# Kernel optimization log

Hardware: AMD Instinct MI355X
Metric: run time of the kernel (lower is better)

The kernel has to match this reference:

```python
import jax, jax.numpy as jnp
import numpy as np

N = 10000        # nodes
E = 320000       # edges (avg degree 32)
W = 256          # width (assert width >= 256)
H = 8            # num_head (RESCALE_EDGE assumed (1,1) -> nhead=8, dhead=32)
D = W // H       # per-head dim
BOND = 33        # EMBED_BOND[0]
BAG = 3          # indices per edge bag
EPS_GN = 1e-5


def setup_inputs() -> dict:
    key = jax.random.key(0)
    ks = jax.random.split(key, 12)
    x = jax.random.normal(ks[0], (N, W), dtype=jnp.float32)
    edge_idx = jax.random.randint(ks[1], (2, E), 0, N)
    edge_attr = jax.random.randint(ks[2], (E, BAG), 0, BOND)
    # node in-degree wrt scatter target edge_idx[1], clamped to >= 1
    deg = jax.ops.segment_sum(jnp.ones((E,), jnp.float32), edge_idx[1], num_segments=N)
    deg = jnp.maximum(deg, 1.0)
    s = 1.0 / np.sqrt(W)
    W_src = jax.random.normal(ks[3], (W, W), dtype=jnp.float32) * s
    W_tgt = jax.random.normal(ks[4], (W, W), dtype=jnp.float32) * s
    emb = jax.random.normal(ks[5], (BOND, W), dtype=jnp.float32) * 0.02
    emb = emb.at[0].set(0.0)  # padding_idx=0 row is zeros
    sd = 1.0 / np.sqrt(D)
    W_gate = jax.random.normal(ks[6], (H, D, D), dtype=jnp.float32) * sd  # grouped conv1d k=1
    W_val = jax.random.normal(ks[7], (H, D, D), dtype=jnp.float32) * sd
    W_post = jax.random.normal(ks[8], (W, W), dtype=jnp.float32) * s
    deg_param = jnp.zeros((W,), jnp.float32) - 0.01  # DegreeLayer degree_init
    return {"x": x, "deg": deg, "edge_idx": edge_idx, "edge_attr": edge_attr,
            "W_src": W_src, "W_tgt": W_tgt, "emb": emb,
            "W_gate": W_gate, "W_val": W_val, "W_post": W_post,
            "deg_param": deg_param}


def reference(x, deg, edge_idx, edge_attr, W_src, W_tgt, emb, W_gate, W_val, W_post, deg_param):
    # src/tgt 1x1 Conv1d == per-node linear, then edge gather
    xs = x @ W_src.T                      # [N, W]
    xt = x @ W_tgt.T                      # [N, W]
    xx = xs[edge_idx[0]] + xt[edge_idx[1]]  # [E, W]

    # EmbeddingBag(mode='mean', padding_idx=0): padded entries excluded
    mask = (edge_attr != 0).astype(xx.dtype)            # [E, BAG]
    bag = jnp.einsum('ebc,eb->ec', emb[edge_attr], mask)  # [E, W]
    cnt = jnp.maximum(mask.sum(-1, keepdims=True), 1.0)
    gate_bias = bag / cnt

    # GroupNorm(H, W, affine=False) over [E, W, 1]
    xg = xx.reshape(-1, H, D)
    mu = xg.mean(-1, keepdims=True)
    var = xg.var(-1, keepdims=True)
    xn = (xg - mu) / jnp.sqrt(var + EPS_GN)              # [E, H, D]

    # gated grouped 1x1 convs (dropout is identity at eval)
    gin = xn + gate_bias.reshape(-1, H, D)
    gate = jax.nn.relu(jnp.einsum('ehd,hfd->ehf', gin, W_gate))
    val = jnp.einsum('ehd,hfd->ehf', xn, W_val)
    act = (gate * val).reshape(-1, W)                    # [E, W]
    out_e = act @ W_post.T                               # [E, W]

    # scatter-sum to nodes, then degree rescale
    agg = jax.ops.segment_sum(out_e, edge_idx[1], num_segments=x.shape[0])
    return jnp.power(deg[:, None], deg_param) * agg      # [N, W]
```

## Files before the change

kernel.cpp:

```cpp
#include <hip/hip_runtime.h>

#define WID 256
#define EPS_GN 1e-5f

typedef __bf16 v8bf __attribute__((ext_vector_type(8)));
typedef __bf16 v2bf __attribute__((ext_vector_type(2)));
typedef float  v4f  __attribute__((ext_vector_type(4)));
typedef float  v2f  __attribute__((ext_vector_type(2)));

__device__ inline unsigned short f2b(float f) {
    unsigned int u = __builtin_bit_cast(unsigned int, f);
    unsigned int r = (u + 0x7fffu + ((u >> 16) & 1u)) >> 16;
    return (unsigned short)r;
}
__device__ inline float lo16(unsigned int u) { return __builtin_bit_cast(float, u << 16); }
__device__ inline float hi16(unsigned int u) { return __builtin_bit_cast(float, u & 0xffff0000u); }
__device__ inline v2f unpk(unsigned int u) {
    v2f r; r.x = lo16(u); r.y = hi16(u); return r;
}

__device__ inline v2f pk_add(v2f a, v2f b) {
    v2f d; asm("v_pk_add_f32 %0, %1, %2" : "=v"(d) : "v"(a), "v"(b)); return d;
}
__device__ inline v2f pk_mul(v2f a, v2f b) {
    v2f d; asm("v_pk_mul_f32 %0, %1, %2" : "=v"(d) : "v"(a), "v"(b)); return d;
}
__device__ inline v2f pk_fma(v2f a, v2f b, v2f c) {
    v2f d; asm("v_pk_fma_f32 %0, %1, %2, %3" : "=v"(d) : "v"(a), "v"(b), "v"(c)); return d;
}

#if __has_builtin(__builtin_amdgcn_cvt_pk_bf16_f32)
__device__ inline unsigned int pkbf(float a, float b) {
    v2bf r = __builtin_amdgcn_cvt_pk_bf16_f32(a, b);
    return __builtin_bit_cast(unsigned int, r);
}
#else
__device__ inline unsigned int pkbf(float a, float b) {
    return (unsigned int)f2b(a) | ((unsigned int)f2b(b) << 16);
}
#endif

#if __has_builtin(__builtin_amdgcn_fdot2_f32_bf16)
__device__ inline float pairsum(unsigned int u, float s) {
    v2bf p = __builtin_bit_cast(v2bf, u);
    v2bf ones = __builtin_bit_cast(v2bf, 0x3f803f80u);
    return __builtin_amdgcn_fdot2_f32_bf16(p, ones, s, false);
}
#else
__device__ inline float pairsum(unsigned int u, float s) {
    return s + lo16(u) + hi16(u);
}
#endif

__global__ void cast_k(const float* __restrict__ Wsrc, const float* __restrict__ Wtgt,
                       const float* __restrict__ Wp, const float* __restrict__ Wg,
                       const float* __restrict__ Wv, const float* __restrict__ emb,
                       const int* __restrict__ eidx,
                       unsigned short* __restrict__ Wsb, unsigned short* __restrict__ Wtb,
                       unsigned short* __restrict__ Wpb, unsigned short* __restrict__ Wgb,
                       unsigned short* __restrict__ Wvb, unsigned short* __restrict__ embWgT,
                       int* __restrict__ cnt, int* __restrict__ ssrc,
                       int* __restrict__ stgt, int* __restrict__ sattr,
                       int N, int BOND, int E, int NT32) {
    int i = blockIdx.x * 256 + threadIdx.x;
    int gsz = gridDim.x * 256;
    for (int j = E + i; j < NT32; j += gsz) { ssrc[j] = 0; stgt[j] = 0; sattr[j] = 0; }
    for (int j = i; j < E; j += gsz) atomicAdd(&cnt[eidx[E + j]], 1);
    {
        const float2* s2 = (const float2*)Wsrc;
        const float2* t2 = (const float2*)Wtgt;
        const float2* p2 = (const float2*)Wp;
        unsigned int* so = (unsigned int*)Wsb;
        unsigned int* to = (unsigned int*)Wtb;
        unsigned int* po = (unsigned int*)Wpb;
        for (int j = i; j < 32768; j += gsz) {
            float2 a = s2[j], b = t2[j], c = p2[j];
            so[j] = pkbf(a.x, a.y); to[j] = pkbf(b.x, b.y); po[j] = pkbf(c.x, c.y);
        }
    }
    {
        const float2* g2 = (const float2*)Wg;
        const float2* v2p = (const float2*)Wv;
        unsigned int* go = (unsigned int*)Wgb;
        unsigned int* vo = (unsigned int*)Wvb;
        for (int j = i; j < 4096; j += gsz) {
            float2 a = g2[j], b = v2p[j];
            go[j] = pkbf(a.x, a.y); vo[j] = pkbf(b.x, b.y);
        }
    }
    for (int j = i; j < 8192; j += gsz) {
        int jr = j >> 5, k = j & 31;
        int kk = k ? k : 32;
        float sacc = 0.f;
        if (kk < BOND) {
            int h = jr >> 5, f = jr & 31;
            const float4* er = (const float4*)(emb + (size_t)kk * WID + h * 32);
            const float4* wr = (const float4*)(Wg + h * 1024 + f * 32);
#pragma unroll
            for (int d = 0; d < 8; d++) {
                float4 e4 = er[d], w4 = wr[d];
                sacc += e4.x * w4.x + e4.y * w4.y + e4.z * w4.z + e4.w * w4.w;
            }
        }
        embWgT[jr * 32 + k] = f2b(sacc);
    }
}

__global__ void scan_k(const int* __restrict__ cnt, int* __restrict__ cur, int N) {
    __shared__ int buf[10240];
    __shared__ int part[1024];
    int t = threadIdx.x;
    int C = (N + 1023) >> 10;
    int M = C << 10;
    for (int i = t; i < M; i += 1024) buf[i] = (i < N) ? cnt[i] : 0;
    __syncthreads();
    int base0 = t * C;
    int s = 0;
    for (int i = 0; i < C; i++) s += buf[base0 + i];
    part[t] = s;
    __syncthreads();
    for (int d = 1; d < 1024; d <<= 1) {
        int v = (t >= d) ? part[t - d] : 0;
        __syncthreads();
        part[t] += v;
        __syncthreads();
    }
    int base = (t == 0) ? 0 : part[t - 1];
    for (int i = 0; i < C; i++) {
        int idx = base0 + i;
        int v = buf[idx];
        buf[idx] = base;
        base += v;
    }
    __syncthreads();
    for (int i = t; i < N; i += 1024) cur[i] = buf[i];
}

__global__ __launch_bounds__(256, 2)
void prepproj_k(const float* __restrict__ x, const unsigned short* __restrict__ Wsb,
                const unsigned short* __restrict__ Wtb, const int* __restrict__ eidx,
                const int* __restrict__ eattr, int* __restrict__ cur,
                int* __restrict__ ssrc, int* __restrict__ stgt, int* __restrict__ sattr,
                unsigned short* __restrict__ xsb, unsigned short* __restrict__ xtb,
                int N, int E, int PB, int AUX) {
    __shared__ unsigned short ab[32 * 264];
    int t = threadIdx.x, b = blockIdx.x;

    if (b >= PB) {
        int atid = (b - PB) * 256 + t, asz = AUX * 256;
        for (int i = atid; i < E; i += asz) {
            int tg = eidx[E + i];
            int p = atomicAdd(&cur[tg], 1);
            ssrc[p] = eidx[i];
            stgt[p] = tg;
            const int* ap = eattr + (size_t)i * 3;
            sattr[p] = (ap[0] & 63) | ((ap[1] & 63) << 6) | ((ap[2] & 63) << 12);
        }
        return;
    }

    int n0 = b * 32;
#pragma unroll
    for (int ch = 0; ch < 8; ch++) {
        int flat = ch * 1024 + t * 4;
        int row = flat >> 8, col = flat & 255;
        int n = n0 + row;
        float4 v = (n < N) ? *(const float4*)&x[(size_t)n * WID + col]
                           : make_float4(0.f, 0.f, 0.f, 0.f);
        *(uint2*)&ab[row * 264 + col] = make_uint2(pkbf(v.x, v.y), pkbf(v.z, v.w));
    }
    __syncthreads();
    int w = t >> 6, lane = t & 63, m = lane & 15, kg = lane >> 4;
#pragma unroll
    for (int pass = 0; pass < 2; pass++) {
        const unsigned short* Wb = pass ? Wtb : Wsb;
        unsigned short* outp = pass ? xtb : xsb;
        v4f acc[2][4];
#pragma unroll
        for (int mt = 0; mt < 2; mt++)
#pragma unroll
            for (int nt = 0; nt < 4; nt++) acc[mt][nt] = (v4f){0.f, 0.f, 0.f, 0.f};
#pragma unroll
        for (int kt = 0; kt < 8; kt++) {
            int k0 = kt * 32 + kg * 8;
            v8bf a0 = *(const v8bf*)&ab[m * 264 + k0];
            v8bf a1 = *(const v8bf*)&ab[(16 + m) * 264 + k0];
#pragma unroll
            for (int nt = 0; nt < 4; nt++) {
                int j = w * 64 + nt * 16 + m;
                v8bf bfr = *(const v8bf*)&Wb[j * 256 + k0];
                acc[0][nt] = __builtin_amdgcn_mfma_f32_16x16x32_bf16(bfr, a0, acc[0][nt], 0, 0, 0);
                acc[1][nt] = __builtin_amdgcn_mfma_f32_16x16x32_bf16(bfr, a1, acc[1][nt], 0, 0, 0);
            }
        }
#pragma unroll
        for (int mt = 0; mt < 2; mt++) {
            int n = n0 + mt * 16 + m;
            if (n < N) {
#pragma unroll
                for (int nt = 0; nt < 4; nt++) {
                    int j0 = w * 64 + nt * 16 + kg * 4;
                    *(uint2*)&outp[(size_t)n * WID + j0] =
                        make_uint2(pkbf(acc[mt][nt][0], acc[mt][nt][1]),
                                   pkbf(acc[mt][nt][2], acc[mt][nt][3]));
                }
            }
        }
    }
}

__global__ __launch_bounds__(256, 8)
void edge_k(const unsigned short* __restrict__ xsb, const unsigned short* __restrict__ xtb,
            const int* __restrict__ ssrc, const int* __restrict__ stgt,
            const int* __restrict__ sattr, const unsigned short* __restrict__ Wgb,
            const unsigned short* __restrict__ Wvb, const unsigned short* __restrict__ embWgT,
            float* __restrict__ aggact, int E, int NT, int PER) {
    __shared__ unsigned short xxb[8704];
    __shared__ unsigned short Mld[32 * 40];
    __shared__ int src_s[32], tgt_s[32];
    __shared__ int segmask_s;

    int tile = (blockIdx.x & 7) * PER + (blockIdx.x >> 3);
    if (tile >= NT) return;
    int t = threadIdx.x;
    int e0 = tile * 32;
    int ne = min(32, E - e0);

    {
        int tgtv = -1;
        if (t < 32) {
            int e = e0 + t;
            src_s[t] = ssrc[e];
            int tg = stgt[e];
            tgt_s[t] = tg;
            int pa = sattr[e];
            uint4* Mr = (uint4*)&Mld[t * 40];
#pragma unroll
            for (int q = 0; q < 4; q++) Mr[q] = make_uint4(0u, 0u, 0u, 0u);
            int a0 = pa & 63, a1 = (pa >> 6) & 63, a2 = (pa >> 12) & 63;
            int c = (a0 != 0) + (a1 != 0) + (a2 != 0);
            float inv = (c > 0) ? 1.f / (float)c : 0.f;
            float wa = inv * (float)(1 + (a1 == a0) + (a2 == a0));
            float wb = inv * (float)(1 + (a2 == a1));
            if (a0) Mld[t * 40 + (a0 & 31)] = f2b(wa);
            if (a1 && a1 != a0) Mld[t * 40 + (a1 & 31)] = f2b(wb);
            if (a2 && a2 != a0 && a2 != a1) Mld[t * 40 + (a2 & 31)] = f2b(inv);
            tgtv = (t < ne) ? tg : -1;
        }
        if (t < 64) {
            int nxt = __shfl_down(tgtv, 1);
            bool flag = (t < ne) && ((t == ne - 1) || (nxt != tgtv));
            unsigned long long bal = __ballot(flag);
            if (t == 0) segmask_s = (int)(unsigned int)bal;
        }
    }
    __syncthreads();

    {
        int e = t >> 3, c = t & 7;
        int sn = src_s[e], g = tgt_s[e];
        const uint4* ps = (const uint4*)(xsb + (size_t)sn * WID);
        const uint4* pt = (const uint4*)(xtb + (size_t)g * WID);
        uint4 us[4], ut[4];
#pragma unroll
        for (int i = 0; i < 4; i++) { us[i] = ps[c + 8 * i]; ut[i] = pt[c + 8 * i]; }
        v2f v2[4][4];
        float sum[4], sq[4];
#pragma unroll
        for (int i = 0; i < 4; i++) {
            const unsigned int* au = (const unsigned int*)&us[i];
            const unsigned int* bu = (const unsigned int*)&ut[i];
            v2f s2 = (v2f){0.f, 0.f}, q2 = (v2f){0.f, 0.f};
#pragma unroll
            for (int q = 0; q < 4; q++) {
                v2f a = pk_add(unpk(au[q]), unpk(bu[q]));
                v2[i][q] = a;
                s2 = pk_add(s2, a);
                q2 = pk_fma(a, a, q2);
            }
            sum[i] = s2.x + s2.y;
            sq[i]  = q2.x + q2.y;
        }
#pragma unroll
        for (int mask = 1; mask <= 2; mask <<= 1)
#pragma unroll
            for (int i = 0; i < 4; i++) {
                sum[i] += __shfl_xor(sum[i], mask);
                sq[i]  += __shfl_xor(sq[i], mask);
            }
#pragma unroll
        for (int i = 0; i < 4; i++) {
            float mu = sum[i] * (1.f / 32.f);
            float var = sq[i] * (1.f / 32.f) - mu * mu;
            float rs = rsqrtf(var + EPS_GN);
            float nmr = -mu * rs;
            v2f rs2 = (v2f){rs, rs}, nm2 = (v2f){nmr, nmr};
            unsigned int pk[4];
#pragma unroll
            for (int q = 0; q < 4; q++) {
                v2f r = pk_fma(v2[i][q], rs2, nm2);
                pk[q] = pkbf(r.x, r.y);
            }
            *(uint4*)&xxb[e * 264 + (c + 8 * i) * 8] = make_uint4(pk[0], pk[1], pk[2], pk[3]);
        }
    }
    __syncthreads();

    {
        int w = t >> 6, lane = t & 63, m = lane & 15, kg = lane >> 4;
        v8bf axn[2][2], aM[2];
#pragma unroll
        for (int mt = 0; mt < 2; mt++) {
            int row = mt * 16 + m;
            axn[0][mt] = *(const v8bf*)&xxb[row * 264 + (w * 2 + 0) * 32 + kg * 8];
            axn[1][mt] = *(const v8bf*)&xxb[row * 264 + (w * 2 + 1) * 32 + kg * 8];
            aM[mt] = *(const v8bf*)&Mld[row * 40 + kg * 8];
        }
        __syncthreads();
        v4f z = {0.f, 0.f, 0.f, 0.f};
#pragma unroll
        for (int hh = 0; hh < 2; hh++) {
            int h = w * 2 + hh;
#pragma unroll
            for (int nt = 0; nt < 2; nt++) {
                int fj = nt * 16 + m;
                int j = h * 32 + fj;
                v8bf bWg = *(const v8bf*)&Wgb[h * 1024 + fj * 32 + kg * 8];
                v8bf bWv = *(const v8bf*)&Wvb[h * 1024 + fj * 32 + kg * 8];
                v8bf bE  = *(const v8bf*)&embWgT[j * 32 + kg * 8];
#pragma unroll
                for (int mt = 0; mt < 2; mt++) {
                    v4f cgm = __builtin_amdgcn_mfma_f32_16x16x32_bf16(axn[hh][mt], bWg, z, 0, 0, 0);
                    cgm = __builtin_amdgcn_mfma_f32_16x16x32_bf16(aM[mt], bE, cgm, 0, 0, 0);
                    v4f cv = __builtin_amdgcn_mfma_f32_16x16x32_bf16(axn[hh][mt], bWv, z, 0, 0, 0);
                    v2f g0 = (v2f){fmaxf(cgm[0], 0.f), fmaxf(cgm[1], 0.f)};
                    v2f g1 = (v2f){fmaxf(cgm[2], 0.f), fmaxf(cgm[3], 0.f)};
                    g0 = pk_mul(g0, (v2f){cv[0], cv[1]});
                    g1 = pk_mul(g1, (v2f){cv[2], cv[3]});
                    int e0i = mt * 16 + kg * 4;
                    *(unsigned int*)&xxb[j * 34 + e0i]     = pkbf(g0.x, g0.y);
                    *(unsigned int*)&xxb[j * 34 + e0i + 2] = pkbf(g1.x, g1.y);
                }
            }
        }
    }
    __syncthreads();

    {
        unsigned int mask = (unsigned int)__builtin_amdgcn_readfirstlane(segmask_s);
        float sum = 0.f;
#pragma unroll
        for (int i = 0; i < 16; i++) {
            unsigned int r = *(const unsigned int*)&xxb[t * 34 + 2 * i];
            if (!((mask >> (2 * i)) & 1)) {
                sum = pairsum(r, sum);
                if ((mask >> (2 * i + 1)) & 1) {
                    int tg = __builtin_amdgcn_readfirstlane(tgt_s[2 * i + 1]);
                    atomicAdd(&aggact[(size_t)tg * WID + t], sum);
                    sum = 0.f;
                }
            } else {
                sum += lo16(r);
                int tg = __builtin_amdgcn_readfirstlane(tgt_s[2 * i]);
                atomicAdd(&aggact[(size_t)tg * WID + t], sum);
                sum = hi16(r);
                if ((mask >> (2 * i + 1)) & 1) {
                    int tg2 = __builtin_amdgcn_readfirstlane(tgt_s[2 * i + 1]);
                    atomicAdd(&aggact[(size_t)tg2 * WID + t], sum);
                    sum = 0.f;
                }
            }
        }
    }
}

__global__ __launch_bounds__(256, 2)
void post_k(const float* __restrict__ aggact, const unsigned short* __restrict__ Wpb,
            const float* __restrict__ deg, const float* __restrict__ dp,
            float* __restrict__ out, int N) {
    __shared__ unsigned short ab[32 * 264];
    __shared__ float degl[32];
    int t = threadIdx.x;
    int n0 = blockIdx.x * 32;
#pragma unroll
    for (int ch = 0; ch < 8; ch++) {
        int flat = ch * 1024 + t * 4;
        int row = flat >> 8, col = flat & 255;
        int n = n0 + row;
        float4 v = (n < N) ? *(const float4*)&aggact[(size_t)n * WID + col]
                           : make_float4(0.f, 0.f, 0.f, 0.f);
        *(uint2*)&ab[row * 264 + col] = make_uint2(pkbf(v.x, v.y), pkbf(v.z, v.w));
    }
    if (t < 32) {
        int n = n0 + t;
        degl[t] = (n < N) ? log2f(deg[n]) : 0.f;
    }
    __syncthreads();
    int w = t >> 6, lane = t & 63, m = lane & 15, kg = lane >> 4;
    v4f acc[2][4];
#pragma unroll
    for (int mt = 0; mt < 2; mt++)
#pragma unroll
        for (int nt = 0; nt < 4; nt++) acc[mt][nt] = (v4f){0.f, 0.f, 0.f, 0.f};
#pragma unroll
    for (int kt = 0; kt < 8; kt++) {
        int k0 = kt * 32 + kg * 8;
        v8bf a0 = *(const v8bf*)&ab[m * 264 + k0];
        v8bf a1 = *(const v8bf*)&ab[(16 + m) * 264 + k0];
#pragma unroll
        for (int nt = 0; nt < 4; nt++) {
            int j = w * 64 + nt * 16 + m;
            v8bf b = *(const v8bf*)&Wpb[j * 256 + k0];
            acc[0][nt] = __builtin_amdgcn_mfma_f32_16x16x32_bf16(b, a0, acc[0][nt], 0, 0, 0);
            acc[1][nt] = __builtin_amdgcn_mfma_f32_16x16x32_bf16(b, a1, acc[1][nt], 0, 0, 0);
        }
    }
#pragma unroll
    for (int mt = 0; mt < 2; mt++) {
        int n = n0 + mt * 16 + m;
        if (n < N) {
            float ld = degl[mt * 16 + m];
#pragma unroll
            for (int nt = 0; nt < 4; nt++) {
                int j0 = w * 64 + nt * 16 + kg * 4;
                float4 dv = *(const float4*)&dp[j0];
                float4 o;
                o.x = exp2f(dv.x * ld) * acc[mt][nt][0];
                o.y = exp2f(dv.y * ld) * acc[mt][nt][1];
                o.z = exp2f(dv.z * ld) * acc[mt][nt][2];
                o.w = exp2f(dv.w * ld) * acc[mt][nt][3];
                *(float4*)&out[(size_t)n * WID + j0] = o;
            }
        }
    }
}

extern "C" void kernel_launch(void* const* d_in, const int* in_sizes, int n_in,
                              void* d_out, int out_size, void* d_ws, size_t ws_size,
                              hipStream_t stream) {
    const float* x    = (const float*)d_in[0];
    const float* deg  = (const float*)d_in[1];
    const int*   eidx = (const int*)d_in[2];
    const int*   eatt = (const int*)d_in[3];
    const float* Wsrc = (const float*)d_in[4];
    const float* Wtgt = (const float*)d_in[5];
    const float* emb  = (const float*)d_in[6];
    const float* Wg   = (const float*)d_in[7];
    const float* Wv   = (const float*)d_in[8];
    const float* Wp   = (const float*)d_in[9];
    const float* dp   = (const float*)d_in[10];
    int N = in_sizes[0] / WID;
    int E = in_sizes[2] / 2;
    int BOND = in_sizes[6] / WID;

    int NT = (E + 31) / 32;
    int NT32 = NT * 32;

    float* ws     = (float*)d_ws;
    float* aggact = ws;
    int*   cnt    = (int*)(aggact + (size_t)N * WID);
    int*   cur    = cnt + N;
    int*   ssrc   = cur + N;
    int*   stgt   = ssrc + NT32;
    int*   sattr  = stgt + NT32;
    unsigned short* xsb = (unsigned short*)(sattr + NT32);
    unsigned short* xtb = xsb + (size_t)N * WID;
    unsigned short* Wsb = xtb + (size_t)N * WID;
    unsigned short* Wtb = Wsb + 65536;
    unsigned short* Wpb = Wtb + 65536;
    unsigned short* Wgb = Wpb + 65536;
    unsigned short* Wvb = Wgb + 8192;
    unsigned short* embWgT = Wvb + 8192;

    int PB = (N + 31) / 32;
    int AUX = 128;
    int PER = (NT + 7) / 8;

    hipMemsetAsync(aggact, 0, (size_t)N * WID * sizeof(float) + (size_t)N * sizeof(int),
                   stream);

    cast_k<<<320, 256, 0, stream>>>(Wsrc, Wtgt, Wp, Wg, Wv, emb, eidx,
                                    Wsb, Wtb, Wpb, Wgb, Wvb, embWgT,
                                    cnt, ssrc, stgt, sattr, N, BOND, E, NT32);
    scan_k<<<1, 1024, 0, stream>>>(cnt, cur, N);
    prepproj_k<<<PB + AUX, 256, 0, stream>>>(x, Wsb, Wtb, eidx, eatt, cur,
                                             ssrc, stgt, sattr, xsb, xtb,
                                             N, E, PB, AUX);
    edge_k<<<PER * 8, 256, 0, stream>>>(xsb, xtb, ssrc, stgt, sattr, Wgb, Wvb, embWgT,
                                        aggact, E, NT, PER);
    post_k<<<PB, 256, 0, stream>>>(aggact, Wpb, deg, dp, (float*)d_out, N);
}
```

Baseline: 211.9 us.

## Pre-swizzle bf16 weights into MFMA fragment order and schedule scatter blocks first

The weight cast kernel now writes W_src, W_tgt and W_post in the exact per-lane MFMA B-fragment order, so the projection and post GEMMs read each fragment as one contiguous 16-byte-per-lane load instead of strided row reads. The edge-sorting (counting-sort scatter) blocks move to the front of the prepproj grid so they are dispatched first, and their count doubles. This aims to improve global load coalescing in the GEMMs and to overlap the atomic-heavy scatter better with the projection work. Both weight consumers must agree on the new layout.

```diff
diff --git a/kernel.cpp b/kernel.cpp
--- a/kernel.cpp
+++ b/kernel.cpp
@@ -66,17 +66,21 @@
     int gsz = gridDim.x * 256;
     for (int j = E + i; j < NT32; j += gsz) { ssrc[j] = 0; stgt[j] = 0; sattr[j] = 0; }
     for (int j = i; j < E; j += gsz) atomicAdd(&cnt[eidx[E + j]], 1);
-    {
-        const float2* s2 = (const float2*)Wsrc;
-        const float2* t2 = (const float2*)Wtgt;
-        const float2* p2 = (const float2*)Wp;
-        unsigned int* so = (unsigned int*)Wsb;
-        unsigned int* to = (unsigned int*)Wtb;
-        unsigned int* po = (unsigned int*)Wpb;
-        for (int j = i; j < 32768; j += gsz) {
-            float2 a = s2[j], b = t2[j], c = p2[j];
-            so[j] = pkbf(a.x, a.y); to[j] = pkbf(b.x, b.y); po[j] = pkbf(c.x, c.y);
-        }
+    for (int j = i; j < 8192; j += gsz) {
+        int lane = j & 63, ktv = (j >> 6) & 7, ntv = (j >> 9) & 3, wv = j >> 11;
+        int src = (wv * 64 + ntv * 16 + (lane & 15)) * 256 + ktv * 32 + (lane >> 4) * 8;
+        const float4* s4 = (const float4*)(Wsrc + src);
+        const float4* t4 = (const float4*)(Wtgt + src);
+        const float4* p4 = (const float4*)(Wp + src);
+        float4 a0 = s4[0], a1 = s4[1];
+        ((uint4*)Wsb)[j] = make_uint4(pkbf(a0.x, a0.y), pkbf(a0.z, a0.w),
+                                      pkbf(a1.x, a1.y), pkbf(a1.z, a1.w));
+        a0 = t4[0]; a1 = t4[1];
+        ((uint4*)Wtb)[j] = make_uint4(pkbf(a0.x, a0.y), pkbf(a0.z, a0.w),
+                                      pkbf(a1.x, a1.y), pkbf(a1.z, a1.w));
+        a0 = p4[0]; a1 = p4[1];
+        ((uint4*)Wpb)[j] = make_uint4(pkbf(a0.x, a0.y), pkbf(a0.z, a0.w),
+                                      pkbf(a1.x, a1.y), pkbf(a1.z, a1.w));
     }
     {
         const float2* g2 = (const float2*)Wg;
@@ -142,12 +146,12 @@
                 const int* __restrict__ eattr, int* __restrict__ cur,
                 int* __restrict__ ssrc, int* __restrict__ stgt, int* __restrict__ sattr,
                 unsigned short* __restrict__ xsb, unsigned short* __restrict__ xtb,
-                int N, int E, int PB, int AUX) {
+                int N, int E, int AUX) {
     __shared__ unsigned short ab[32 * 264];
     int t = threadIdx.x, b = blockIdx.x;
 
-    if (b >= PB) {
-        int atid = (b - PB) * 256 + t, asz = AUX * 256;
+    if (b < AUX) {
+        int atid = b * 256 + t, asz = AUX * 256;
         for (int i = atid; i < E; i += asz) {
             int tg = eidx[E + i];
             int p = atomicAdd(&cur[tg], 1);
@@ -159,7 +163,7 @@
         return;
     }
 
-    int n0 = b * 32;
+    int n0 = (b - AUX) * 32;
 #pragma unroll
     for (int ch = 0; ch < 8; ch++) {
         int flat = ch * 1024 + t * 4;
@@ -187,8 +191,7 @@
             v8bf a1 = *(const v8bf*)&ab[(16 + m) * 264 + k0];
 #pragma unroll
             for (int nt = 0; nt < 4; nt++) {
-                int j = w * 64 + nt * 16 + m;
-                v8bf bfr = *(const v8bf*)&Wb[j * 256 + k0];
+                v8bf bfr = *(const v8bf*)&Wb[(((w * 4 + nt) * 8 + kt) * 64 + lane) * 8];
                 acc[0][nt] = __builtin_amdgcn_mfma_f32_16x16x32_bf16(bfr, a0, acc[0][nt], 0, 0, 0);
                 acc[1][nt] = __builtin_amdgcn_mfma_f32_16x16x32_bf16(bfr, a1, acc[1][nt], 0, 0, 0);
             }
@@ -409,8 +412,7 @@
         v8bf a1 = *(const v8bf*)&ab[(16 + m) * 264 + k0];
 #pragma unroll
         for (int nt = 0; nt < 4; nt++) {
-            int j = w * 64 + nt * 16 + m;
-            v8bf b = *(const v8bf*)&Wpb[j * 256 + k0];
+            v8bf b = *(const v8bf*)&Wpb[(((w * 4 + nt) * 8 + kt) * 64 + lane) * 8];
             acc[0][nt] = __builtin_amdgcn_mfma_f32_16x16x32_bf16(b, a0, acc[0][nt], 0, 0, 0);
             acc[1][nt] = __builtin_amdgcn_mfma_f32_16x16x32_bf16(b, a1, acc[1][nt], 0, 0, 0);
         }
@@ -473,7 +475,7 @@
     unsigned short* embWgT = Wvb + 8192;
 
     int PB = (N + 31) / 32;
-    int AUX = 128;
+    int AUX = 256;
     int PER = (NT + 7) / 8;
 
     hipMemsetAsync(aggact, 0, (size_t)N * WID * sizeof(float) + (size_t)N * sizeof(int),
@@ -483,9 +485,9 @@
                                     Wsb, Wtb, Wpb, Wgb, Wvb, embWgT,
                                     cnt, ssrc, stgt, sattr, N, BOND, E, NT32);
     scan_k<<<1, 1024, 0, stream>>>(cnt, cur, N);
-    prepproj_k<<<PB + AUX, 256, 0, stream>>>(x, Wsb, Wtb, eidx, eatt, cur,
+    prepproj_k<<<AUX + PB, 256, 0, stream>>>(x, Wsb, Wtb, eidx, eatt, cur,
                                              ssrc, stgt, sattr, xsb, xtb,
-                                             N, E, PB, AUX);
+                                             N, E, AUX);
     edge_k<<<PER * 8, 256, 0, stream>>>(xsb, xtb, ssrc, stgt, sattr, Wgb, Wvb, embWgT,
                                         aggact, E, NT, PER);
     post_k<<<PB, 256, 0, stream>>>(aggact, Wpb, deg, dp, (float*)d_out, N);
```

Result: slower. 217.4 us (+2.6%).
